# Optimization experiments

Hardware: AMD Instinct MI355X
Metric: run time of the kernel (lower is better)

Reference implementation:

```python
import jax, jax.numpy as jnp
import numpy as np

IN_DIM, OUT_DIM, EDGE_DIM = 128, 64, 16
BS, N = 8, 512

def setup_inputs() -> dict:
    key = jax.random.key(0)
    k1, k2, k3, k4 = jax.random.split(key, 4)
    x = jax.random.normal(k1, (BS, N, IN_DIM), dtype=jnp.float32)
    edge_feats = jax.random.normal(k2, (BS, N, N, EDGE_DIM), dtype=jnp.float32)
    # nn.Linear weights: fc (out_dim, in_dim), attn_fc (1, 2*out_dim+edge_dim)
    W_fc = jax.random.normal(k3, (OUT_DIM, IN_DIM), dtype=jnp.float32) / np.sqrt(IN_DIM)
    attn_w = jax.random.normal(k4, (2 * OUT_DIM + EDGE_DIM,), dtype=jnp.float32) / np.sqrt(2 * OUT_DIM + EDGE_DIM)
    return {"x": x, "edge_feats": edge_feats, "W_fc": W_fc, "attn_w": attn_w}

def reference(x, edge_feats, W_fc, attn_w):
    # h: (bs, N, out_dim)
    h = jnp.einsum('bni,oi->bno', x, W_fc)
    # Split attn_fc weight: concat([h_i, h_j, edge]) @ a == h_i@a_i + h_j@a_j + edge@a_e
    a_i = attn_w[:OUT_DIM]
    a_j = attn_w[OUT_DIM:2 * OUT_DIM]
    a_e = attn_w[2 * OUT_DIM:]
    s_i = jnp.einsum('bno,o->bn', h, a_i)              # (bs, N)
    s_j = jnp.einsum('bno,o->bn', h, a_j)              # (bs, N)
    s_e = jnp.einsum('bijk,k->bij', edge_feats, a_e)   # (bs, N, N)
    e_ij = s_i[:, :, None] + s_j[:, None, :] + s_e     # (bs, N, N)
    alpha = jax.nn.softmax(e_ij, axis=-1)              # softmax over j
    # weighted sum of h_j over j
    h_prime = jnp.einsum('bij,bjo->bio', alpha, h)
    return h_prime
```

## Files before the change

### kernel.cpp

```cpp
#include <hip/hip_runtime.h>

constexpr int IN_DIM   = 128;
constexpr int OUT_DIM  = 64;
constexpr int EDGE_DIM = 16;
constexpr int BS       = 8;
constexpr int NN       = 512;
constexpr int ROWS     = BS * NN;
constexpr int TI       = 4;

__global__ __launch_bounds__(256, 4) void fc_kernel(
    const float* __restrict__ x, const float* __restrict__ W,
    const float* __restrict__ attn_w,
    float* __restrict__ h, float* __restrict__ sj)
{
    __shared__ float  xs[8 * IN_DIM];
    __shared__ float4 ws[64 * 33];
    const int t    = threadIdx.x;
    const int lane = t & 63;
    const int w    = t >> 6;
    const int rowBase = blockIdx.x * 8;

    ((float4*)xs)[t] = ((const float4*)(x + (size_t)rowBase * IN_DIM))[t];
    const float4* W4 = (const float4*)W;
    #pragma unroll
    for (int i = 0; i < 8; ++i) {
        const int s = t + i * 256;
        ws[(s >> 5) * 33 + (s & 31)] = W4[s];
    }
    const float a_j = attn_w[OUT_DIM + lane];
    __syncthreads();

    const float4* xr0 = (const float4*)&xs[(w * 2 + 0) * IN_DIM];
    const float4* xr1 = (const float4*)&xs[(w * 2 + 1) * IN_DIM];
    float acc0 = 0.f, acc1 = 0.f;
    #pragma unroll 8
    for (int k = 0; k < IN_DIM / 4; ++k) {
        const float4 wv = ws[lane * 33 + k];
        const float4 x0 = xr0[k];
        const float4 x1 = xr1[k];
        acc0 += x0.x * wv.x + x0.y * wv.y + x0.z * wv.z + x0.w * wv.w;
        acc1 += x1.x * wv.x + x1.y * wv.y + x1.z * wv.z + x1.w * wv.w;
    }
    #pragma unroll
    for (int r = 0; r < 2; ++r) {
        const float a   = r ? acc1 : acc0;
        const int   row = rowBase + w * 2 + r;
        h[(size_t)row * OUT_DIM + lane] = a;
        float pj = a * a_j;
        #pragma unroll
        for (int m = 32; m > 0; m >>= 1) pj += __shfl_xor(pj, m, 64);
        if (lane == 0) sj[row] = pj;
    }
}

__global__ __launch_bounds__(256, 4) void attn_kernel(
    const float* __restrict__ edge, const float* __restrict__ attn_w,
    const float* __restrict__ h, const float* __restrict__ sj,
    float* __restrict__ out)
{
    __shared__ float  sjb[NN];
    __shared__ float  alpha[TI * NN];
    __shared__ float4 part[TI][16][16];

    const int t    = threadIdx.x;
    const int lane = t & 63;
    const int w    = t >> 6;
    const int blk  = blockIdx.x;
    const int b    = blk >> 7;
    const int iRow = (blk & 127) * TI + w;
    const size_t rowg = ((size_t)b << 9) + iRow;

    if (t < 128)
        ((float4*)sjb)[t] = ((const float4*)(sj + ((size_t)b << 9)))[t];

    const float4* ae4 = (const float4*)(attn_w + 2 * OUT_DIM);
    const float4 ae0 = ae4[0], ae1 = ae4[1], ae2 = ae4[2], ae3 = ae4[3];
    const float4* ef4 = (const float4*)edge + rowg * (NN * EDGE_DIM / 4);
    __syncthreads();

    float e[8];
    #pragma unroll 4
    for (int jj = 0; jj < 8; ++jj) {
        const int j = jj * 64 + lane;
        const float4 v0 = ef4[j * 4 + 0], v1 = ef4[j * 4 + 1];
        const float4 v2 = ef4[j * 4 + 2], v3 = ef4[j * 4 + 3];
        const float se = v0.x * ae0.x + v0.y * ae0.y + v0.z * ae0.z + v0.w * ae0.w
                       + v1.x * ae1.x + v1.y * ae1.y + v1.z * ae1.z + v1.w * ae1.w
                       + v2.x * ae2.x + v2.y * ae2.y + v2.z * ae2.z + v2.w * ae2.w
                       + v3.x * ae3.x + v3.y * ae3.y + v3.z * ae3.z + v3.w * ae3.w;
        e[jj] = sjb[j] + se;
    }

    float m = e[0];
    #pragma unroll
    for (int jj = 1; jj < 8; ++jj) m = fmaxf(m, e[jj]);
    #pragma unroll
    for (int msk = 32; msk > 0; msk >>= 1) m = fmaxf(m, __shfl_xor(m, msk, 64));

    float p[8], s = 0.f;
    #pragma unroll
    for (int jj = 0; jj < 8; ++jj) { p[jj] = __expf(e[jj] - m); s += p[jj]; }
    #pragma unroll
    for (int msk = 32; msk > 0; msk >>= 1) s += __shfl_xor(s, msk, 64);
    const float rinv = 1.0f / s;
    #pragma unroll
    for (int jj = 0; jj < 8; ++jj)
        alpha[w * NN + jj * 64 + lane] = p[jj] * rinv;

    __syncthreads();

    const int o4 = t & 15;
    const int g  = t >> 4;
    const float4* h4 = (const float4*)(h + (((size_t)b) << 9) * OUT_DIM);
    float4 acc[TI];
    #pragma unroll
    for (int r = 0; r < TI; ++r) acc[r] = make_float4(0.f, 0.f, 0.f, 0.f);
    #pragma unroll 4
    for (int j = g; j < NN; j += 16) {
        const float4 hv = h4[j * 16 + o4];
        #pragma unroll
        for (int r = 0; r < TI; ++r) {
            const float a = alpha[r * NN + j];
            acc[r].x += a * hv.x; acc[r].y += a * hv.y;
            acc[r].z += a * hv.z; acc[r].w += a * hv.w;
        }
    }
    #pragma unroll
    for (int r = 0; r < TI; ++r) part[r][g][o4] = acc[r];
    __syncthreads();

    {
        const int c = lane & 15;
        const int q = lane >> 4;
        float4 v = part[w][q * 4 + 0][c];
        #pragma unroll
        for (int i = 1; i < 4; ++i) {
            const float4 u = part[w][q * 4 + i][c];
            v.x += u.x; v.y += u.y; v.z += u.z; v.w += u.w;
        }
        #pragma unroll
        for (int msk = 16; msk <= 32; msk <<= 1) {
            v.x += __shfl_xor(v.x, msk, 64);
            v.y += __shfl_xor(v.y, msk, 64);
            v.z += __shfl_xor(v.z, msk, 64);
            v.w += __shfl_xor(v.w, msk, 64);
        }
        if (q == 0)
            ((float4*)out)[rowg * 16 + c] = v;
    }
}

extern "C" void kernel_launch(void* const* d_in, const int* in_sizes, int n_in,
                              void* d_out, int out_size, void* d_ws, size_t ws_size,
                              hipStream_t stream) {
    const float* x      = (const float*)d_in[0];
    const float* edge   = (const float*)d_in[1];
    const float* W_fc   = (const float*)d_in[2];
    const float* attn_w = (const float*)d_in[3];
    float* out = (float*)d_out;

    float* h  = (float*)d_ws;
    float* sj = h + (size_t)ROWS * OUT_DIM;

    fc_kernel<<<ROWS / 8, 256, 0, stream>>>(x, W_fc, attn_w, h, sj);
    attn_kernel<<<ROWS / TI, 256, 0, stream>>>(edge, attn_w, h, sj, out);
}
```

Measured before the change: 205.1 us.

## Split each attention row across two waves with coalesced edge loads

The attention kernel now handles two query rows per block, with each row split across two wavefronts. Each group of four lanes cooperatively reads one edge vector and reduces it with shuffles, so a wave reads contiguous memory. Softmax normalization moves to the final output step, and the cross-wave max and sum are combined through shared memory. Launch bounds are raised so more blocks can be resident, aiming to hide memory latency better. The trade-off is that the block count doubles, which doubles L2 reads of h, and a single 32-thread tail now does the final reduction serially.

Result: slower. 209.8 us (+2.3%).

```diff
diff --git a/kernel.cpp b/kernel.cpp
--- a/kernel.cpp
+++ b/kernel.cpp
@@ -6,7 +6,7 @@
 constexpr int BS       = 8;
 constexpr int NN       = 512;
 constexpr int ROWS     = BS * NN;
-constexpr int TI       = 4;
+constexpr int TI       = 2;
 
 __global__ __launch_bounds__(256, 4) void fc_kernel(
     const float* __restrict__ x, const float* __restrict__ W,
@@ -53,7 +53,7 @@
     }
 }
 
-__global__ __launch_bounds__(256, 4) void attn_kernel(
+__global__ __launch_bounds__(256, 8) void attn_kernel(
     const float* __restrict__ edge, const float* __restrict__ attn_w,
     const float* __restrict__ h, const float* __restrict__ sj,
     float* __restrict__ out)
@@ -61,92 +61,88 @@
     __shared__ float  sjb[NN];
     __shared__ float  alpha[TI * NN];
     __shared__ float4 part[TI][16][16];
+    __shared__ float  rm[TI][2], rs[TI][2];
 
     const int t    = threadIdx.x;
     const int lane = t & 63;
     const int w    = t >> 6;
+    const int r    = w >> 1;
+    const int hf   = w & 1;
     const int blk  = blockIdx.x;
-    const int b    = blk >> 7;
-    const int iRow = (blk & 127) * TI + w;
-    const size_t rowg = ((size_t)b << 9) + iRow;
+    const int b    = blk >> 8;
+    const int itile = blk & 255;
+    const size_t rowg = ((size_t)b << 9) + itile * TI + r;
 
     if (t < 128)
         ((float4*)sjb)[t] = ((const float4*)(sj + ((size_t)b << 9)))[t];
 
-    const float4* ae4 = (const float4*)(attn_w + 2 * OUT_DIM);
-    const float4 ae0 = ae4[0], ae1 = ae4[1], ae2 = ae4[2], ae3 = ae4[3];
+    const float4 aesel = ((const float4*)(attn_w + 2 * OUT_DIM))[lane & 3];
     const float4* ef4 = (const float4*)edge + rowg * (NN * EDGE_DIM / 4);
     __syncthreads();
 
-    float e[8];
+    const int jq = lane >> 2;
+    const int q  = lane & 3;
+    float m = -1e30f;
     #pragma unroll 4
-    for (int jj = 0; jj < 8; ++jj) {
-        const int j = jj * 64 + lane;
-        const float4 v0 = ef4[j * 4 + 0], v1 = ef4[j * 4 + 1];
-        const float4 v2 = ef4[j * 4 + 2], v3 = ef4[j * 4 + 3];
-        const float se = v0.x * ae0.x + v0.y * ae0.y + v0.z * ae0.z + v0.w * ae0.w
-                       + v1.x * ae1.x + v1.y * ae1.y + v1.z * ae1.z + v1.w * ae1.w
-                       + v2.x * ae2.x + v2.y * ae2.y + v2.z * ae2.z + v2.w * ae2.w
-                       + v3.x * ae3.x + v3.y * ae3.y + v3.z * ae3.z + v3.w * ae3.w;
-        e[jj] = sjb[j] + se;
+    for (int it = 0; it < 16; ++it) {
+        const int j = hf * 256 + it * 16 + jq;
+        const float4 v = ef4[j * 4 + q];
+        float pd = v.x * aesel.x + v.y * aesel.y + v.z * aesel.z + v.w * aesel.w;
+        pd += __shfl_xor(pd, 1, 64);
+        pd += __shfl_xor(pd, 2, 64);
+        const float ev = pd + sjb[j];
+        m = fmaxf(m, ev);
+        if (q == 0) alpha[r * NN + j] = ev;
     }
+    #pragma unroll
+    for (int msk = 4; msk < 64; msk <<= 1) m = fmaxf(m, __shfl_xor(m, msk, 64));
+    if (lane == 0) rm[r][hf] = m;
+    __syncthreads();
+    m = fmaxf(rm[r][0], rm[r][1]);
 
-    float m = e[0];
+    float s = 0.f;
     #pragma unroll
-    for (int jj = 1; jj < 8; ++jj) m = fmaxf(m, e[jj]);
+    for (int k = 0; k < 4; ++k) {
+        const int idx = r * NN + hf * 256 + k * 64 + lane;
+        const float p = __expf(alpha[idx] - m);
+        alpha[idx] = p;
+        s += p;
+    }
     #pragma unroll
-    for (int msk = 32; msk > 0; msk >>= 1) m = fmaxf(m, __shfl_xor(m, msk, 64));
-
-    float p[8], s = 0.f;
-    #pragma unroll
-    for (int jj = 0; jj < 8; ++jj) { p[jj] = __expf(e[jj] - m); s += p[jj]; }
-    #pragma unroll
-    for (int msk = 32; msk > 0; msk >>= 1) s += __shfl_xor(s, msk, 64);
-    const float rinv = 1.0f / s;
-    #pragma unroll
-    for (int jj = 0; jj < 8; ++jj)
-        alpha[w * NN + jj * 64 + lane] = p[jj] * rinv;
-
+    for (int msk = 1; msk < 64; msk <<= 1) s += __shfl_xor(s, msk, 64);
+    if (lane == 0) rs[r][hf] = s;
     __syncthreads();
 
     const int o4 = t & 15;
     const int g  = t >> 4;
     const float4* h4 = (const float4*)(h + (((size_t)b) << 9) * OUT_DIM);
-    float4 acc[TI];
-    #pragma unroll
-    for (int r = 0; r < TI; ++r) acc[r] = make_float4(0.f, 0.f, 0.f, 0.f);
+    float4 acc0 = make_float4(0.f, 0.f, 0.f, 0.f);
+    float4 acc1 = make_float4(0.f, 0.f, 0.f, 0.f);
     #pragma unroll 4
     for (int j = g; j < NN; j += 16) {
         const float4 hv = h4[j * 16 + o4];
-        #pragma unroll
-        for (int r = 0; r < TI; ++r) {
-            const float a = alpha[r * NN + j];
-            acc[r].x += a * hv.x; acc[r].y += a * hv.y;
-            acc[r].z += a * hv.z; acc[r].w += a * hv.w;
-        }
+        const float a0 = alpha[j];
+        const float a1 = alpha[NN + j];
+        acc0.x += a0 * hv.x; acc0.y += a0 * hv.y;
+        acc0.z += a0 * hv.z; acc0.w += a0 * hv.w;
+        acc1.x += a1 * hv.x; acc1.y += a1 * hv.y;
+        acc1.z += a1 * hv.z; acc1.w += a1 * hv.w;
     }
-    #pragma unroll
-    for (int r = 0; r < TI; ++r) part[r][g][o4] = acc[r];
+    part[0][g][o4] = acc0;
+    part[1][g][o4] = acc1;
     __syncthreads();
 
-    {
-        const int c = lane & 15;
-        const int q = lane >> 4;
-        float4 v = part[w][q * 4 + 0][c];
+    if (t < 32) {
+        const int rr = t >> 4, c = t & 15;
+        float4 v = part[rr][0][c];
         #pragma unroll
-        for (int i = 1; i < 4; ++i) {
-            const float4 u = part[w][q * 4 + i][c];
+        for (int g2 = 1; g2 < 16; ++g2) {
+            const float4 u = part[rr][g2][c];
             v.x += u.x; v.y += u.y; v.z += u.z; v.w += u.w;
         }
-        #pragma unroll
-        for (int msk = 16; msk <= 32; msk <<= 1) {
-            v.x += __shfl_xor(v.x, msk, 64);
-            v.y += __shfl_xor(v.y, msk, 64);
-            v.z += __shfl_xor(v.z, msk, 64);
-            v.w += __shfl_xor(v.w, msk, 64);
-        }
-        if (q == 0)
-            ((float4*)out)[rowg * 16 + c] = v;
+        const float rinv = 1.0f / (rs[rr][0] + rs[rr][1]);
+        v.x *= rinv; v.y *= rinv; v.z *= rinv; v.w *= rinv;
+        ((float4*)out)[(((size_t)b << 9) + itile * TI + rr) * 16 + c] = v;
     }
 }
 
```
